# Optimization experiments

Measured on AMD Instinct MI355X. Metric: run time of the kernel, lower is better.

Reference implementation:

```python
import jax, jax.numpy as jnp
import numpy as np
import math

N_HEAD = 9
N_KV_HEAD = 3
HEAD_DIM = 64
ROPE_THETA = 100000.0


def _rope_cos_sin(seq_len, dim, theta):
    inv_freq = 1.0 / (theta ** (jnp.arange(0, dim, 2, dtype=jnp.float32) / dim))  # (dim//2,)
    t = jnp.arange(seq_len, dtype=jnp.float32)
    ang = jnp.outer(t, inv_freq)  # (T, dim//2)
    return jnp.cos(ang), jnp.sin(ang)


def _apply_rope(x, cos, sin):
    # x: (B, H, T, D); pairs are interleaved along D (torch view_as_complex on (..., D//2, 2))
    B, H, T, D = x.shape
    xr = x.reshape(B, H, T, D // 2, 2)
    x0, x1 = xr[..., 0], xr[..., 1]
    c = cos[None, None, :, :]
    s = sin[None, None, :, :]
    out0 = x0 * c - x1 * s
    out1 = x0 * s + x1 * c
    return jnp.stack([out0, out1], axis=-1).reshape(B, H, T, D)


def setup_inputs() -> dict:
    key = jax.random.key(0)
    ks = jax.random.split(key, 5)
    B, T, C = 4, 2048, 576
    scale_in = 1.0 / math.sqrt(C)
    return {
        "x": jax.random.normal(ks[0], (B, T, C), dtype=jnp.float32),
        "wq": jax.random.normal(ks[1], (N_HEAD * HEAD_DIM, C), dtype=jnp.float32) * scale_in,
        "wk": jax.random.normal(ks[2], (N_KV_HEAD * HEAD_DIM, C), dtype=jnp.float32) * scale_in,
        "wv": jax.random.normal(ks[3], (N_KV_HEAD * HEAD_DIM, C), dtype=jnp.float32) * scale_in,
        "wo": jax.random.normal(ks[4], (C, N_HEAD * HEAD_DIM), dtype=jnp.float32) * scale_in,
    }


def reference(x, wq, wk, wv, wo):
    B, T, C = x.shape
    n_rep = N_HEAD // N_KV_HEAD

    q = (x @ wq.T).reshape(B, T, N_HEAD, HEAD_DIM).transpose(0, 2, 1, 3)      # (B,Hq,T,D)
    k = (x @ wk.T).reshape(B, T, N_KV_HEAD, HEAD_DIM).transpose(0, 2, 1, 3)   # (B,Hkv,T,D)
    v = (x @ wv.T).reshape(B, T, N_KV_HEAD, HEAD_DIM).transpose(0, 2, 1, 3)

    cos, sin = _rope_cos_sin(T, HEAD_DIM, ROPE_THETA)
    q = _apply_rope(q, cos, sin)
    k = _apply_rope(k, cos, sin)

    # GQA: broadcast each KV head across n_rep query heads without materializing copies
    qg = q.reshape(B, N_KV_HEAD, n_rep, T, HEAD_DIM)
    att = jnp.einsum("bgrtd,bgsd->bgrts", qg, k) * (1.0 / math.sqrt(HEAD_DIM))  # (B,Hkv,rep,T,T)
    causal = jnp.tril(jnp.ones((T, T), dtype=bool))
    att = jnp.where(causal[None, None, None, :, :], att, -jnp.inf)
    att = jax.nn.softmax(att, axis=-1)
    y = jnp.einsum("bgrts,bgsd->bgrtd", att, v)                                # (B,Hkv,rep,T,D)
    y = y.reshape(B, N_HEAD, T, HEAD_DIM).transpose(0, 2, 1, 3).reshape(B, T, N_HEAD * HEAD_DIM)
    return y @ wo.T
```

## Files before the change

### kernel.cpp

```cpp
#include <hip/hip_runtime.h>
#include <stdint.h>

typedef __attribute__((ext_vector_type(8))) short bf16x8;
typedef __attribute__((ext_vector_type(16))) float f32x16;

#define MFMA32(a, b, c) __builtin_amdgcn_mfma_f32_32x32x16_bf16(a, b, c, 0, 0, 0)

#define BB 4
#define TT 2048
#define CC 576
#define NH 9
#define NKV 3
#define HD 64
#define MM (BB * TT)
#define NQKV 960

#define QSC 0.18033688011112042f

__device__ __forceinline__ unsigned short f2bf(float f) {
  union { float f; uint32_t u; } v; v.f = f;
  uint32_t u = v.u;
  uint32_t r = (u + 0x7fffu + ((u >> 16) & 1u)) >> 16;
  return (unsigned short)r;
}

__device__ __forceinline__ void gl16(const void* g, void* l) {
  __builtin_amdgcn_global_load_lds(
      (const __attribute__((address_space(1))) unsigned int*)g,
      (__attribute__((address_space(3))) unsigned int*)l, 16, 0, 0);
}

__device__ __forceinline__ float fexp2(float x) {
  float r;
  asm("v_exp_f32 %0, %1" : "=v"(r) : "v"(x));
  return r;
}

__global__ __launch_bounds__(256) void prep_kernel(
    const float* __restrict__ x, const float* __restrict__ wq,
    const float* __restrict__ wk, const float* __restrict__ wv,
    const float* __restrict__ wo,
    unsigned short* __restrict__ xh, unsigned short* __restrict__ wqkv,
    unsigned short* __restrict__ woh, float* __restrict__ tc,
    float* __restrict__ ts) {
  const int NX4 = MM * CC / 4;
  const int NW4 = NQKV * CC / 4;
  const int NO4 = CC * CC / 4;
  const int NT = TT * 32;
  const int total = NX4 + NW4 + NO4 + NT;
  for (int i = blockIdx.x * blockDim.x + threadIdx.x; i < total;
       i += gridDim.x * blockDim.x) {
    if (i < NX4) {
      float4 v = ((const float4*)x)[i];
      ushort4 o;
      o.x = f2bf(v.x); o.y = f2bf(v.y); o.z = f2bf(v.z); o.w = f2bf(v.w);
      ((ushort4*)xh)[i] = o;
    } else if (i < NX4 + NW4) {
      int j = i - NX4;
      int n = (j * 4) / CC;
      const float* src = (n < 576) ? wq + j * 4
                       : (n < 768) ? wk + j * 4 - 576 * CC
                                   : wv + j * 4 - 768 * CC;
      float4 v = *(const float4*)src;
      ushort4 o;
      o.x = f2bf(v.x); o.y = f2bf(v.y); o.z = f2bf(v.z); o.w = f2bf(v.w);
      ((ushort4*)wqkv)[j] = o;
    } else if (i < NX4 + NW4 + NO4) {
      int j = i - NX4 - NW4;
      float4 v = ((const float4*)wo)[j];
      ushort4 o;
      o.x = f2bf(v.x); o.y = f2bf(v.y); o.z = f2bf(v.z); o.w = f2bf(v.w);
      ((ushort4*)woh)[j] = o;
    } else {
      int j = i - NX4 - NW4 - NO4;
      int t = j >> 5, pi = j & 31;
      double invf = pow(100000.0, -(double)(2 * pi) / 64.0);
      double ang = (double)t * invf;
      tc[j] = (float)cos(ang);
      ts[j] = (float)sin(ang);
    }
  }
}

__global__ __launch_bounds__(512, 4) void gemm_qkv(
    const unsigned short* __restrict__ xh, const unsigned short* __restrict__ wqkv,
    const float* __restrict__ tc, const float* __restrict__ ts,
    unsigned short* __restrict__ qb, unsigned short* __restrict__ kst,
    unsigned short* __restrict__ vst) {
  const int l = threadIdx.x & 63, w = threadIdx.x >> 6;
  const int ln = l & 31, hi = l >> 5;
  const int bm = blockIdx.y * 256, bn = blockIdx.x * 64;

  __shared__ unsigned short als[2][16384];
  __shared__ unsigned short bls[2][4096];

  int asrc[4];
#pragma unroll
  for (int i = 0; i < 4; ++i)
    asrc[i] = (bm + w * 32 + i * 8 + (l >> 3)) * CC + ((l & 7) ^ ((l >> 3) & 7)) * 8;
  const int bsrc = (bn + w * 8 + (l >> 3)) * CC + ((l & 7) ^ ((l >> 3) & 7)) * 8;

  f32x16 acc0, acc1;
#pragma unroll
  for (int r = 0; r < 16; ++r) { acc0[r] = 0.f; acc1[r] = 0.f; }

#pragma unroll
  for (int i = 0; i < 4; ++i) gl16(xh + asrc[i], (char*)&als[0][0] + w * 4096 + i * 1024);
  gl16(wqkv + bsrc, (char*)&bls[0][0] + w * 1024);

  int cur = 0;
  for (int t = 0; t < 9; ++t) {
    if (t + 1 < 9) {
      const int k0 = (t + 1) * 64;
#pragma unroll
      for (int i = 0; i < 4; ++i)
        gl16(xh + asrc[i] + k0, (char*)&als[cur ^ 1][0] + w * 4096 + i * 1024);
      gl16(wqkv + bsrc + k0, (char*)&bls[cur ^ 1][0] + w * 1024);
      asm volatile("s_waitcnt vmcnt(5)" ::: "memory");
    } else {
      asm volatile("s_waitcnt vmcnt(0)" ::: "memory");
    }
    __builtin_amdgcn_s_barrier();
    __builtin_amdgcn_sched_barrier(0);

    const char* ab = (const char*)&als[cur][0];
    const char* bb = (const char*)&bls[cur][0];
    __builtin_amdgcn_s_setprio(1);
#pragma unroll
    for (int ks = 0; ks < 4; ++ks) {
      const int ch = (((ks * 2 + hi) ^ (ln & 7)) << 4);
      bf16x8 af = *(const bf16x8*)(ab + (w * 32 + ln) * 128 + ch);
      bf16x8 b0 = *(const bf16x8*)(bb + ln * 128 + ch);
      bf16x8 b1 = *(const bf16x8*)(bb + (32 + ln) * 128 + ch);
      acc0 = MFMA32(af, b0, acc0);
      acc1 = MFMA32(af, b1, acc1);
    }
    __builtin_amdgcn_s_setprio(0);

    __builtin_amdgcn_sched_barrier(0);
    __builtin_amdgcn_s_barrier();
    cur ^= 1;
  }

#pragma unroll
  for (int n32 = 0; n32 < 2; ++n32) {
    const int col = bn + n32 * 32 + ln;
    const int d = col & 63;
#pragma unroll
    for (int r = 0; r < 16; ++r) {
      const int m = bm + w * 32 + (r & 3) + 8 * (r >> 2) + 4 * hi;
      float v = n32 ? acc1[r] : acc0[r];
      float partner = __shfl_xor(v, 1);
      const int bi = m >> 11, t = m & 2047;
      if (col < 768) {
        const int pi = d >> 1;
        const float c = tc[t * 32 + pi], s = ts[t * 32 + pi];
        v = (d & 1) ? (partner * s + v * c) : (v * c - partner * s);
      }
      if (col < 576) {
        const int h = col >> 6;
        qb[(((size_t)bi * NH + h) * TT + t) * HD + d] = f2bf(v * QSC);
      } else if (col < 768) {
        const int h = (col - 576) >> 6;
        const size_t head = (size_t)bi * NKV + h;
        const int tt = t & 63;
        kst[(head * 32 + (t >> 6)) * 4096 + ((d >> 4) * 2 + (tt >> 5)) * 512
            + ((((d >> 3) & 1) << 5) + (tt & 31)) * 8 + (d & 7)] = f2bf(v);
      } else {
        const int h = (col - 768) >> 6;
        const size_t head = (size_t)bi * NKV + h;
        const int tt = t & 63;
        vst[(head * 32 + (t >> 6)) * 4096 + ((tt >> 4) * 2 + (d >> 5)) * 512
            + ((((tt >> 3) & 1) << 5) + (d & 31)) * 8 + (tt & 7)] = f2bf(v);
      }
    }
  }
}

__global__ __launch_bounds__(512, 4) void attn_kernel(
    const unsigned short* __restrict__ qbuf, const unsigned short* __restrict__ kst,
    const unsigned short* __restrict__ vst, unsigned short* __restrict__ yb) {
  const int jx = blockIdx.x, kvh = blockIdx.y, b = blockIdx.z;
  const int j = jx % 13, hr = jx / 13;
  const int h = kvh * 3 + hr;
  const int l = threadIdx.x & 63;
  const int w8 = threadIdx.x >> 6;
  const int g = w8 >> 2;
  const int wq = w8 & 3;
  const int ln = l & 31, hi = l >> 5;
  const size_t head = (size_t)b * NKV + kvh;

  const int qt0 = 15 - j;
  const int qt1 = (j >= 9 && j <= 11) ? (j - 9) : -1;
  const int m0 = qt0 + 1;
  const int m1 = (qt1 >= 0) ? qt1 + 1 : 0;
  const int tot = m0 + m1;

  __shared__ unsigned short kls[2][2][4096];
  __shared__ unsigned short vls[2][2][4096];
  __shared__ float licomb[256];

  const unsigned short* qptr = qbuf + ((size_t)b * NH + h) * TT * HD;
  const int row0 = qt0 * 128 + wq * 32 + ln;
  const int row1 = ((qt1 >= 0) ? qt1 : 0) * 128 + wq * 32 + ln;

  bf16x8 qf0[4], qf1[4], qc[4];
#pragma unroll
  for (int ds = 0; ds < 4; ++ds) {
    qf0[ds] = *(const bf16x8*)(qptr + (size_t)row0 * HD + ds * 16 + hi * 8);
    qf1[ds] = *(const bf16x8*)(qptr + (size_t)row1 * HD + ds * 16 + hi * 8);
  }
  qc[0] = qf0[0]; qc[1] = qf0[1]; qc[2] = qf0[2]; qc[3] = qf0[3];
  int qt_c = qt0, qrow_c = row0, nt_c = m0;

  const char* kgb = (const char*)(kst + head * 32 * 4096);
  const char* vgb = (const char*)(vst + head * 32 * 4096);

  f32x16 o0, o1, fzero;
  float ls[16];
#pragma unroll
  for (int r = 0; r < 16; ++r) { o0[r] = 0.f; o1[r] = 0.f; ls[r] = 0.f; fzero[r] = 0.f; }

  {
    const size_t tb = (size_t)g * 8192;
#pragma unroll
    for (int i2 = 0; i2 < 2; ++i2) {
      const int off = wq * 2048 + i2 * 1024;
      gl16(kgb + tb + off + l * 16, (char*)&kls[g][0][0] + off);
      gl16(vgb + tb + off + l * 16, (char*)&vls[g][0][0] + off);
    }
  }

  int jt = 0;

  for (int it = 0; it < tot; ++it) {
    if (it + 1 < tot) {
      const int f = it + 1;
      const int u = (f < m0) ? f : f - m0;
      const size_t tb = (size_t)(2 * u + g) * 8192;
      char* kl = (char*)&kls[g][(it + 1) & 1][0];
      char* vl = (char*)&vls[g][(it + 1) & 1][0];
#pragma unroll
      for (int i2 = 0; i2 < 2; ++i2) {
        const int off = wq * 2048 + i2 * 1024;
        gl16(kgb + tb + off + l * 16, kl + off);
        gl16(vgb + tb + off + l * 16, vl + off);
      }
      asm volatile("s_waitcnt vmcnt(4)" ::: "memory");
    } else {
      asm volatile("s_waitcnt vmcnt(0)" ::: "memory");
    }
    __builtin_amdgcn_s_barrier();
    __builtin_amdgcn_sched_barrier(0);

    const char* kb = (const char*)&kls[g][it & 1][0];
    const char* vb = (const char*)&vls[g][it & 1][0];

    f32x16 s0, s1;
    __builtin_amdgcn_s_setprio(1);
    {
      bf16x8 k0 = *(const bf16x8*)(kb + 0 * 1024 + l * 16);
      bf16x8 k1 = *(const bf16x8*)(kb + 1 * 1024 + l * 16);
      s0 = MFMA32(k0, qc[0], fzero);
      s1 = MFMA32(k1, qc[0], fzero);
    }
#pragma unroll
    for (int ds = 1; ds < 4; ++ds) {
      bf16x8 k0 = *(const bf16x8*)(kb + (ds * 2 + 0) * 1024 + l * 16);
      bf16x8 k1 = *(const bf16x8*)(kb + (ds * 2 + 1) * 1024 + l * 16);
      s0 = MFMA32(k0, qc[ds], s0);
      s1 = MFMA32(k1, qc[ds], s1);
    }
    __builtin_amdgcn_s_setprio(0);

    const bool segEnd = (jt == qt_c);
    if (segEnd) {
      const int kvt = 2 * qt_c + g;
#pragma unroll
      for (int r = 0; r < 16; ++r) {
        const int kg = kvt * 64 + (r & 3) + 8 * (r >> 2) + 4 * hi;
        if (kg > qrow_c) s0[r] = -1e30f;
        if (kg + 32 > qrow_c) s1[r] = -1e30f;
      }
    }

#pragma unroll
    for (int r = 0; r < 16; ++r) {
      s0[r] = fexp2(s0[r]);
      s1[r] = fexp2(s1[r]);
    }
#pragma unroll
    for (int r = 0; r < 16; ++r) ls[r] += s0[r] + s1[r];

    unsigned int pa[4][4];
#pragma unroll
    for (int t = 0; t < 2; ++t) {
#pragma unroll
      for (int m = 0; m < 2; ++m) {
        float p0 = t ? s1[8 * m + 0] : s0[8 * m + 0];
        float p1 = t ? s1[8 * m + 1] : s0[8 * m + 1];
        float p2 = t ? s1[8 * m + 2] : s0[8 * m + 2];
        float p3 = t ? s1[8 * m + 3] : s0[8 * m + 3];
        float p4 = t ? s1[8 * m + 4] : s0[8 * m + 4];
        float p5 = t ? s1[8 * m + 5] : s0[8 * m + 5];
        float p6 = t ? s1[8 * m + 6] : s0[8 * m + 6];
        float p7 = t ? s1[8 * m + 7] : s0[8 * m + 7];
        unsigned int w0, w1, w2, w3;
        asm("v_cvt_pk_bf16_f32 %0, %1, %2" : "=v"(w0) : "v"(p0), "v"(p1));
        asm("v_cvt_pk_bf16_f32 %0, %1, %2" : "=v"(w1) : "v"(p2), "v"(p3));
        asm("v_cvt_pk_bf16_f32 %0, %1, %2" : "=v"(w2) : "v"(p4), "v"(p5));
        asm("v_cvt_pk_bf16_f32 %0, %1, %2" : "=v"(w3) : "v"(p6), "v"(p7));
        asm("v_permlane32_swap_b32 %0, %1" : "+v"(w0), "+v"(w2));
        asm("v_permlane32_swap_b32 %0, %1" : "+v"(w1), "+v"(w3));
        pa[2 * t + m][0] = w0; pa[2 * t + m][1] = w1;
        pa[2 * t + m][2] = w2; pa[2 * t + m][3] = w3;
      }
    }

    __builtin_amdgcn_s_setprio(1);
#pragma unroll
    for (int ks = 0; ks < 4; ++ks) {
      union { unsigned int u[4]; bf16x8 v; } cvt;
      cvt.u[0] = pa[ks][0]; cvt.u[1] = pa[ks][1];
      cvt.u[2] = pa[ks][2]; cvt.u[3] = pa[ks][3];
      bf16x8 v0 = *(const bf16x8*)(vb + (ks * 2 + 0) * 1024 + l * 16);
      bf16x8 v1 = *(const bf16x8*)(vb + (ks * 2 + 1) * 1024 + l * 16);
      o0 = MFMA32(cvt.v, v0, o0);
      o1 = MFMA32(cvt.v, v1, o1);
    }
    __builtin_amdgcn_s_setprio(0);

    if (segEnd) {
#pragma unroll
      for (int st = 8; st >= 1; st >>= 1)
#pragma unroll
        for (int r = 0; r < 8; ++r)
          if (r < st) ls[r] += ls[r + st];
      const float tm0 = ls[0] + __shfl_xor(ls[0], 32);
      char* chunk;
      {
        const int buf = it & 1;
        chunk = (char*)((wq == 0) ? &kls[0][buf][0]
               : (wq == 1) ? &vls[0][buf][0]
               : (wq == 2) ? &kls[1][buf][0]
                           : &vls[1][buf][0]);
      }
      __syncthreads();
      if (g == 1) {
#pragma unroll
        for (int r = 0; r < 16; ++r) {
          *(float*)(chunk + r * 256 + l * 4) = o0[r];
          *(float*)(chunk + (16 + r) * 256 + l * 4) = o1[r];
        }
        licomb[wq * 64 + l] = tm0;
      }
      __syncthreads();
      if (g == 0) {
#pragma unroll
        for (int r = 0; r < 16; ++r) {
          o0[r] += *(const float*)(chunk + r * 256 + l * 4);
          o1[r] += *(const float*)(chunk + (16 + r) * 256 + l * 4);
        }
        const float li = tm0 + licomb[wq * 64 + l];
        const float inv = 1.0f / li;
#pragma unroll
        for (int r = 0; r < 16; ++r) {
          const int cr = (r & 3) + 8 * (r >> 2) + 4 * hi;
          const float ir = __shfl(inv, cr);
          const int t = qt_c * 128 + wq * 32 + cr;
          unsigned short* yp = yb + ((size_t)b * TT + t) * CC + h * HD;
          yp[ln] = f2bf(o0[r] * ir);
          yp[32 + ln] = f2bf(o1[r] * ir);
        }
      }
#pragma unroll
      for (int r = 0; r < 16; ++r) { o0[r] = 0.f; o1[r] = 0.f; ls[r] = 0.f; }
    }

    __builtin_amdgcn_sched_barrier(0);
    __builtin_amdgcn_s_barrier();
    __builtin_amdgcn_sched_barrier(0);

    ++jt;
    if (jt == nt_c && it + 1 < tot) {
      jt = 0;
      qt_c = qt1; qrow_c = row1; nt_c = m1;
      qc[0] = qf1[0]; qc[1] = qf1[1]; qc[2] = qf1[2]; qc[3] = qf1[3];
    }
  }
}

__global__ __launch_bounds__(512, 4) void gemm_out(
    const unsigned short* __restrict__ yb, const unsigned short* __restrict__ woh,
    float* __restrict__ out) {
  const int l = threadIdx.x & 63, w = threadIdx.x >> 6;
  const int ln = l & 31, hi = l >> 5;
  const int bm = blockIdx.y * 256, bn = blockIdx.x * 64;

  __shared__ unsigned short als[2][16384];
  __shared__ unsigned short bls[2][4096];

  int asrc[4];
#pragma unroll
  for (int i = 0; i < 4; ++i)
    asrc[i] = (bm + w * 32 + i * 8 + (l >> 3)) * CC + ((l & 7) ^ ((l >> 3) & 7)) * 8;
  const int bsrc = (bn + w * 8 + (l >> 3)) * CC + ((l & 7) ^ ((l >> 3) & 7)) * 8;

  f32x16 acc0, acc1;
#pragma unroll
  for (int r = 0; r < 16; ++r) { acc0[r] = 0.f; acc1[r] = 0.f; }

#pragma unroll
  for (int i = 0; i < 4; ++i) gl16(yb + asrc[i], (char*)&als[0][0] + w * 4096 + i * 1024);
  gl16(woh + bsrc, (char*)&bls[0][0] + w * 1024);

  int cur = 0;
  for (int t = 0; t < 9; ++t) {
    if (t + 1 < 9) {
      const int k0 = (t + 1) * 64;
#pragma unroll
      for (int i = 0; i < 4; ++i)
        gl16(yb + asrc[i] + k0, (char*)&als[cur ^ 1][0] + w * 4096 + i * 1024);
      gl16(woh + bsrc + k0, (char*)&bls[cur ^ 1][0] + w * 1024);
      asm volatile("s_waitcnt vmcnt(5)" ::: "memory");
    } else {
      asm volatile("s_waitcnt vmcnt(0)" ::: "memory");
    }
    __builtin_amdgcn_s_barrier();
    __builtin_amdgcn_sched_barrier(0);

    const char* ab = (const char*)&als[cur][0];
    const char* bb = (const char*)&bls[cur][0];
    __builtin_amdgcn_s_setprio(1);
#pragma unroll
    for (int ks = 0; ks < 4; ++ks) {
      const int ch = (((ks * 2 + hi) ^ (ln & 7)) << 4);
      bf16x8 af = *(const bf16x8*)(ab + (w * 32 + ln) * 128 + ch);
      bf16x8 b0 = *(const bf16x8*)(bb + ln * 128 + ch);
      bf16x8 b1 = *(const bf16x8*)(bb + (32 + ln) * 128 + ch);
      acc0 = MFMA32(af, b0, acc0);
      acc1 = MFMA32(af, b1, acc1);
    }
    __builtin_amdgcn_s_setprio(0);

    __builtin_amdgcn_sched_barrier(0);
    __builtin_amdgcn_s_barrier();
    cur ^= 1;
  }

#pragma unroll
  for (int n32 = 0; n32 < 2; ++n32) {
    const int col = bn + n32 * 32 + ln;
#pragma unroll
    for (int r = 0; r < 16; ++r) {
      const int m = bm + w * 32 + (r & 3) + 8 * (r >> 2) + 4 * hi;
      out[(size_t)m * CC + col] = n32 ? acc1[r] : acc0[r];
    }
  }
}

extern "C" void kernel_launch(void* const* d_in, const int* in_sizes, int n_in,
                              void* d_out, int out_size, void* d_ws, size_t ws_size,
                              hipStream_t stream) {
  const float* x = (const float*)d_in[0];
  const float* wq = (const float*)d_in[1];
  const float* wk = (const float*)d_in[2];
  const float* wv = (const float*)d_in[3];
  const float* wo = (const float*)d_in[4];
  float* out = (float*)d_out;

  char* ws = (char*)d_ws;
  unsigned short* xh = (unsigned short*)ws;    ws += (size_t)MM * CC * 2;
  unsigned short* wqkv = (unsigned short*)ws;  ws += (size_t)NQKV * CC * 2;
  unsigned short* woh = (unsigned short*)ws;   ws += (size_t)CC * CC * 2;
  float* tc = (float*)ws;                      ws += (size_t)TT * 32 * 4;
  float* tsn = (float*)ws;                     ws += (size_t)TT * 32 * 4;
  unsigned short* qbuf = (unsigned short*)ws;  ws += (size_t)BB * NH * TT * HD * 2;
  unsigned short* kst = (unsigned short*)ws;   ws += (size_t)BB * NKV * TT * HD * 2;
  unsigned short* vst = (unsigned short*)ws;   ws += (size_t)BB * NKV * HD * TT * 2;
  unsigned short* yb = (unsigned short*)ws;    ws += (size_t)MM * CC * 2;

  prep_kernel<<<dim3(2048), dim3(256), 0, stream>>>(x, wq, wk, wv, wo, xh, wqkv, woh, tc, tsn);
  gemm_qkv<<<dim3(NQKV / 64, MM / 256), dim3(512), 0, stream>>>(xh, wqkv, tc, tsn, qbuf, kst, vst);
  attn_kernel<<<dim3(39, NKV, BB), dim3(512), 0, stream>>>(qbuf, kst, vst, yb);
  gemm_out<<<dim3(CC / 64, MM / 256), dim3(512), 0, stream>>>(yb, woh, out);
}
```

Baseline: 98.93 us.

## Split long causal attention rows across blocks with partial-sum epilogue kernel

Replaces the paired query-tile scheduling (one long plus one short tile per block) with a table of 20 bins, where the four longest query tiles (12-15) are split into two KV ranges handled by separate blocks. Split blocks write unnormalized partial outputs and row sums to a scratch buffer aliased over the now-dead xh workspace, and a new epilogue kernel combines and normalizes them. The goal is better load balance and more blocks (720 vs 468) for the causal workload, at the cost of an extra kernel launch and fp32 scratch traffic. The workspace layout is reordered so woh is not overwritten by the scratch.

```diff
diff --git a/kernel.cpp b/kernel.cpp
--- a/kernel.cpp
+++ b/kernel.cpp
@@ -35,6 +35,10 @@
   asm("v_exp_f32 %0, %1" : "=v"(r) : "v"(x));
   return r;
 }
+
+__device__ const signed char BQT[20] = {11,10,9,8,15,15,14,7,14,13,13,12,6,12,5,4,3,2,1,0};
+__device__ const signed char BLO[20] = {0,0,0,0,0,8,0,0,8,0,7,0,0,7,0,0,0,0,0,0};
+__device__ const signed char BHI[20] = {12,11,10,9,8,16,8,8,15,7,14,7,7,13,6,5,4,3,2,1};
 
 __global__ __launch_bounds__(256) void prep_kernel(
     const float* __restrict__ x, const float* __restrict__ wq,
@@ -179,39 +183,30 @@
 
 __global__ __launch_bounds__(512, 4) void attn_kernel(
     const unsigned short* __restrict__ qbuf, const unsigned short* __restrict__ kst,
-    const unsigned short* __restrict__ vst, unsigned short* __restrict__ yb) {
-  const int jx = blockIdx.x, kvh = blockIdx.y, b = blockIdx.z;
-  const int j = jx % 13, hr = jx / 13;
+    const unsigned short* __restrict__ vst, unsigned short* __restrict__ yb,
+    float* __restrict__ pscr) {
+  const int x = blockIdx.x, kvh = blockIdx.y, b = blockIdx.z;
+  const int bin = x / 3, hr = x % 3;
   const int h = kvh * 3 + hr;
+  const int qt = BQT[bin], klo = BLO[bin], khi = BHI[bin];
   const int l = threadIdx.x & 63;
   const int w8 = threadIdx.x >> 6;
   const int g = w8 >> 2;
   const int wq = w8 & 3;
-  const int ln = l & 31, hi = l >> 5;
+  const int ln = l & 31, hb = l >> 5;
   const size_t head = (size_t)b * NKV + kvh;
-
-  const int qt0 = 15 - j;
-  const int qt1 = (j >= 9 && j <= 11) ? (j - 9) : -1;
-  const int m0 = qt0 + 1;
-  const int m1 = (qt1 >= 0) ? qt1 + 1 : 0;
-  const int tot = m0 + m1;
 
   __shared__ unsigned short kls[2][2][4096];
   __shared__ unsigned short vls[2][2][4096];
   __shared__ float licomb[256];
 
   const unsigned short* qptr = qbuf + ((size_t)b * NH + h) * TT * HD;
-  const int row0 = qt0 * 128 + wq * 32 + ln;
-  const int row1 = ((qt1 >= 0) ? qt1 : 0) * 128 + wq * 32 + ln;
-
-  bf16x8 qf0[4], qf1[4], qc[4];
-#pragma unroll
-  for (int ds = 0; ds < 4; ++ds) {
-    qf0[ds] = *(const bf16x8*)(qptr + (size_t)row0 * HD + ds * 16 + hi * 8);
-    qf1[ds] = *(const bf16x8*)(qptr + (size_t)row1 * HD + ds * 16 + hi * 8);
-  }
-  qc[0] = qf0[0]; qc[1] = qf0[1]; qc[2] = qf0[2]; qc[3] = qf0[3];
-  int qt_c = qt0, qrow_c = row0, nt_c = m0;
+  const int qrow = qt * 128 + wq * 32 + ln;
+
+  bf16x8 qc[4];
+#pragma unroll
+  for (int ds = 0; ds < 4; ++ds)
+    qc[ds] = *(const bf16x8*)(qptr + (size_t)qrow * HD + ds * 16 + hb * 8);
 
   const char* kgb = (const char*)(kst + head * 32 * 4096);
   const char* vgb = (const char*)(vst + head * 32 * 4096);
@@ -222,7 +217,7 @@
   for (int r = 0; r < 16; ++r) { o0[r] = 0.f; o1[r] = 0.f; ls[r] = 0.f; fzero[r] = 0.f; }
 
   {
-    const size_t tb = (size_t)g * 8192;
+    const size_t tb = (size_t)(2 * klo + g) * 8192;
 #pragma unroll
     for (int i2 = 0; i2 < 2; ++i2) {
       const int off = wq * 2048 + i2 * 1024;
@@ -231,15 +226,12 @@
     }
   }
 
-  int jt = 0;
-
-  for (int it = 0; it < tot; ++it) {
-    if (it + 1 < tot) {
-      const int f = it + 1;
-      const int u = (f < m0) ? f : f - m0;
-      const size_t tb = (size_t)(2 * u + g) * 8192;
-      char* kl = (char*)&kls[g][(it + 1) & 1][0];
-      char* vl = (char*)&vls[g][(it + 1) & 1][0];
+  for (int u = klo; u < khi; ++u) {
+    const int it2 = u - klo;
+    if (u + 1 < khi) {
+      const size_t tb = (size_t)(2 * (u + 1) + g) * 8192;
+      char* kl = (char*)&kls[g][(it2 + 1) & 1][0];
+      char* vl = (char*)&vls[g][(it2 + 1) & 1][0];
 #pragma unroll
       for (int i2 = 0; i2 < 2; ++i2) {
         const int off = wq * 2048 + i2 * 1024;
@@ -253,8 +245,8 @@
     __builtin_amdgcn_s_barrier();
     __builtin_amdgcn_sched_barrier(0);
 
-    const char* kb = (const char*)&kls[g][it & 1][0];
-    const char* vb = (const char*)&vls[g][it & 1][0];
+    const char* kb = (const char*)&kls[g][it2 & 1][0];
+    const char* vb = (const char*)&vls[g][it2 & 1][0];
 
     f32x16 s0, s1;
     __builtin_amdgcn_s_setprio(1);
@@ -273,14 +265,13 @@
     }
     __builtin_amdgcn_s_setprio(0);
 
-    const bool segEnd = (jt == qt_c);
-    if (segEnd) {
-      const int kvt = 2 * qt_c + g;
+    if (u == qt) {
+      const int kvt = 2 * qt + g;
 #pragma unroll
       for (int r = 0; r < 16; ++r) {
-        const int kg = kvt * 64 + (r & 3) + 8 * (r >> 2) + 4 * hi;
-        if (kg > qrow_c) s0[r] = -1e30f;
-        if (kg + 32 > qrow_c) s1[r] = -1e30f;
+        const int kg = kvt * 64 + (r & 3) + 8 * (r >> 2) + 4 * hb;
+        if (kg > qrow) s0[r] = -1e30f;
+        if (kg + 32 > qrow) s1[r] = -1e30f;
       }
     }
 
@@ -330,63 +321,87 @@
     }
     __builtin_amdgcn_s_setprio(0);
 
-    if (segEnd) {
-#pragma unroll
-      for (int st = 8; st >= 1; st >>= 1)
-#pragma unroll
-        for (int r = 0; r < 8; ++r)
-          if (r < st) ls[r] += ls[r + st];
-      const float tm0 = ls[0] + __shfl_xor(ls[0], 32);
-      char* chunk;
-      {
-        const int buf = it & 1;
-        chunk = (char*)((wq == 0) ? &kls[0][buf][0]
-               : (wq == 1) ? &vls[0][buf][0]
-               : (wq == 2) ? &kls[1][buf][0]
-                           : &vls[1][buf][0]);
-      }
-      __syncthreads();
-      if (g == 1) {
-#pragma unroll
-        for (int r = 0; r < 16; ++r) {
-          *(float*)(chunk + r * 256 + l * 4) = o0[r];
-          *(float*)(chunk + (16 + r) * 256 + l * 4) = o1[r];
-        }
-        licomb[wq * 64 + l] = tm0;
-      }
-      __syncthreads();
-      if (g == 0) {
-#pragma unroll
-        for (int r = 0; r < 16; ++r) {
-          o0[r] += *(const float*)(chunk + r * 256 + l * 4);
-          o1[r] += *(const float*)(chunk + (16 + r) * 256 + l * 4);
-        }
-        const float li = tm0 + licomb[wq * 64 + l];
-        const float inv = 1.0f / li;
-#pragma unroll
-        for (int r = 0; r < 16; ++r) {
-          const int cr = (r & 3) + 8 * (r >> 2) + 4 * hi;
-          const float ir = __shfl(inv, cr);
-          const int t = qt_c * 128 + wq * 32 + cr;
-          unsigned short* yp = yb + ((size_t)b * TT + t) * CC + h * HD;
-          yp[ln] = f2bf(o0[r] * ir);
-          yp[32 + ln] = f2bf(o1[r] * ir);
-        }
-      }
-#pragma unroll
-      for (int r = 0; r < 16; ++r) { o0[r] = 0.f; o1[r] = 0.f; ls[r] = 0.f; }
-    }
-
     __builtin_amdgcn_sched_barrier(0);
     __builtin_amdgcn_s_barrier();
     __builtin_amdgcn_sched_barrier(0);
-
-    ++jt;
-    if (jt == nt_c && it + 1 < tot) {
-      jt = 0;
-      qt_c = qt1; qrow_c = row1; nt_c = m1;
-      qc[0] = qf1[0]; qc[1] = qf1[1]; qc[2] = qf1[2]; qc[3] = qf1[3];
-    }
+  }
+
+#pragma unroll
+  for (int st = 8; st >= 1; st >>= 1)
+#pragma unroll
+    for (int r = 0; r < 8; ++r)
+      if (r < st) ls[r] += ls[r + st];
+  const float tm0 = ls[0] + __shfl_xor(ls[0], 32);
+  char* chunk;
+  {
+    const int buf = (khi - 1 - klo) & 1;
+    chunk = (char*)((wq == 0) ? &kls[0][buf][0]
+           : (wq == 1) ? &vls[0][buf][0]
+           : (wq == 2) ? &kls[1][buf][0]
+                       : &vls[1][buf][0]);
+  }
+  __syncthreads();
+  if (g == 1) {
+#pragma unroll
+    for (int r = 0; r < 16; ++r) {
+      *(float*)(chunk + r * 256 + l * 4) = o0[r];
+      *(float*)(chunk + (16 + r) * 256 + l * 4) = o1[r];
+    }
+    licomb[wq * 64 + l] = tm0;
+  }
+  __syncthreads();
+  if (g == 0) {
+#pragma unroll
+    for (int r = 0; r < 16; ++r) {
+      o0[r] += *(const float*)(chunk + r * 256 + l * 4);
+      o1[r] += *(const float*)(chunk + (16 + r) * 256 + l * 4);
+    }
+    const float li = tm0 + licomb[wq * 64 + l];
+    if (qt >= 12) {
+      const int half = (klo == 0) ? 0 : 1;
+      float* po = pscr + ((((size_t)(b * NH + h) * 4 + (qt - 12)) * 2 + half)) * 8320;
+#pragma unroll
+      for (int r = 0; r < 16; ++r) {
+        const int cr = (r & 3) + 8 * (r >> 2) + 4 * hb;
+        po[(wq * 32 + cr) * 64 + ln] = o0[r];
+        po[(wq * 32 + cr) * 64 + 32 + ln] = o1[r];
+      }
+      if (hb == 0) po[8192 + wq * 32 + ln] = li;
+    } else {
+      const float inv = 1.0f / li;
+#pragma unroll
+      for (int r = 0; r < 16; ++r) {
+        const int cr = (r & 3) + 8 * (r >> 2) + 4 * hb;
+        const float ir = __shfl(inv, cr);
+        const int t = qt * 128 + wq * 32 + cr;
+        unsigned short* yp = yb + ((size_t)b * TT + t) * CC + h * HD;
+        yp[ln] = f2bf(o0[r] * ir);
+        yp[32 + ln] = f2bf(o1[r] * ir);
+      }
+    }
+  }
+}
+
+__global__ __launch_bounds__(256) void attn_epilogue(
+    const float* __restrict__ pscr, unsigned short* __restrict__ yb) {
+  const int q4 = blockIdx.x, h = blockIdx.y, b = blockIdx.z;
+  const int qt = q4 + 12;
+  const float* p0 = pscr + (((size_t)(b * NH + h) * 4 + q4) * 2 + 0) * 8320;
+  const float* p1 = p0 + 8320;
+#pragma unroll
+  for (int e = 0; e < 8; ++e) {
+    const int i4 = e * 256 + threadIdx.x;
+    const int row = i4 >> 4;
+    const float inv = 1.0f / (p0[8192 + row] + p1[8192 + row]);
+    float4 a = ((const float4*)p0)[i4];
+    float4 c = ((const float4*)p1)[i4];
+    ushort4 o;
+    o.x = f2bf((a.x + c.x) * inv);
+    o.y = f2bf((a.y + c.y) * inv);
+    o.z = f2bf((a.z + c.z) * inv);
+    o.w = f2bf((a.w + c.w) * inv);
+    const int col = (i4 & 15) * 4;
+    *(ushort4*)(yb + ((size_t)b * TT + qt * 128 + row) * CC + h * HD + col) = o;
   }
 }
 
@@ -470,11 +485,12 @@
   float* out = (float*)d_out;
 
   char* ws = (char*)d_ws;
+  float* pscr = (float*)d_ws;
   unsigned short* xh = (unsigned short*)ws;    ws += (size_t)MM * CC * 2;
   unsigned short* wqkv = (unsigned short*)ws;  ws += (size_t)NQKV * CC * 2;
-  unsigned short* woh = (unsigned short*)ws;   ws += (size_t)CC * CC * 2;
   float* tc = (float*)ws;                      ws += (size_t)TT * 32 * 4;
   float* tsn = (float*)ws;                     ws += (size_t)TT * 32 * 4;
+  unsigned short* woh = (unsigned short*)ws;   ws += (size_t)CC * CC * 2;
   unsigned short* qbuf = (unsigned short*)ws;  ws += (size_t)BB * NH * TT * HD * 2;
   unsigned short* kst = (unsigned short*)ws;   ws += (size_t)BB * NKV * TT * HD * 2;
   unsigned short* vst = (unsigned short*)ws;   ws += (size_t)BB * NKV * HD * TT * 2;
@@ -482,6 +498,7 @@
 
   prep_kernel<<<dim3(2048), dim3(256), 0, stream>>>(x, wq, wk, wv, wo, xh, wqkv, woh, tc, tsn);
   gemm_qkv<<<dim3(NQKV / 64, MM / 256), dim3(512), 0, stream>>>(xh, wqkv, tc, tsn, qbuf, kst, vst);
-  attn_kernel<<<dim3(39, NKV, BB), dim3(512), 0, stream>>>(qbuf, kst, vst, yb);
+  attn_kernel<<<dim3(60, NKV, BB), dim3(512), 0, stream>>>(qbuf, kst, vst, yb, pscr);
+  attn_epilogue<<<dim3(4, NH, BB), dim3(256), 0, stream>>>(pscr, yb);
   gemm_out<<<dim3(CC / 64, MM / 256), dim3(512), 0, stream>>>(yb, woh, out);
 }
```

Result: slower. 102.6 us (+3.8%).

## Simplify attention to one query tile per block with single KV stream

Applied to the files above, without the earlier changes.

Replaces the two-group split-KV attention blocks, which paired query tiles for load balancing and merged partial outputs through shared memory, with 256-thread blocks that each own one 128-row query tile and walk all KV tiles serially. Per-wave causal skipping avoids computing tiles fully above the diagonal, and the cross-group LDS reduction and extra syncs are removed. The cost is less intra-block KV parallelism and causal load imbalance across blocks, now left to the hardware scheduler with a larger grid of 576 blocks. Workspace buffer order is also shuffled.

```diff
diff --git a/kernel.cpp b/kernel.cpp
--- a/kernel.cpp
+++ b/kernel.cpp
@@ -177,41 +177,27 @@
   }
 }
 
-__global__ __launch_bounds__(512, 4) void attn_kernel(
+__global__ __launch_bounds__(256, 5) void attn_kernel(
     const unsigned short* __restrict__ qbuf, const unsigned short* __restrict__ kst,
     const unsigned short* __restrict__ vst, unsigned short* __restrict__ yb) {
-  const int jx = blockIdx.x, kvh = blockIdx.y, b = blockIdx.z;
-  const int j = jx % 13, hr = jx / 13;
-  const int h = kvh * 3 + hr;
-  const int l = threadIdx.x & 63;
-  const int w8 = threadIdx.x >> 6;
-  const int g = w8 >> 2;
-  const int wq = w8 & 3;
-  const int ln = l & 31, hi = l >> 5;
+  const int qt = 15 - blockIdx.x, h = blockIdx.y, b = blockIdx.z;
+  const int l = threadIdx.x & 63, wq = threadIdx.x >> 6;
+  const int ln = l & 31, hb = l >> 5;
+  const int kvh = h / 3;
   const size_t head = (size_t)b * NKV + kvh;
-
-  const int qt0 = 15 - j;
-  const int qt1 = (j >= 9 && j <= 11) ? (j - 9) : -1;
-  const int m0 = qt0 + 1;
-  const int m1 = (qt1 >= 0) ? qt1 + 1 : 0;
-  const int tot = m0 + m1;
-
-  __shared__ unsigned short kls[2][2][4096];
-  __shared__ unsigned short vls[2][2][4096];
-  __shared__ float licomb[256];
+  const int nt = 2 * qt + 2;
+
+  __shared__ unsigned short kls[2][4096];
+  __shared__ unsigned short vls[2][4096];
 
   const unsigned short* qptr = qbuf + ((size_t)b * NH + h) * TT * HD;
-  const int row0 = qt0 * 128 + wq * 32 + ln;
-  const int row1 = ((qt1 >= 0) ? qt1 : 0) * 128 + wq * 32 + ln;
-
-  bf16x8 qf0[4], qf1[4], qc[4];
-#pragma unroll
-  for (int ds = 0; ds < 4; ++ds) {
-    qf0[ds] = *(const bf16x8*)(qptr + (size_t)row0 * HD + ds * 16 + hi * 8);
-    qf1[ds] = *(const bf16x8*)(qptr + (size_t)row1 * HD + ds * 16 + hi * 8);
-  }
-  qc[0] = qf0[0]; qc[1] = qf0[1]; qc[2] = qf0[2]; qc[3] = qf0[3];
-  int qt_c = qt0, qrow_c = row0, nt_c = m0;
+  const int qrow = qt * 128 + wq * 32 + ln;
+  const int wmax = qt * 128 + wq * 32 + 31;
+
+  bf16x8 qc[4];
+#pragma unroll
+  for (int ds = 0; ds < 4; ++ds)
+    qc[ds] = *(const bf16x8*)(qptr + (size_t)qrow * HD + ds * 16 + hb * 8);
 
   const char* kgb = (const char*)(kst + head * 32 * 4096);
   const char* vgb = (const char*)(vst + head * 32 * 4096);
@@ -221,25 +207,18 @@
 #pragma unroll
   for (int r = 0; r < 16; ++r) { o0[r] = 0.f; o1[r] = 0.f; ls[r] = 0.f; fzero[r] = 0.f; }
 
-  {
-    const size_t tb = (size_t)g * 8192;
-#pragma unroll
-    for (int i2 = 0; i2 < 2; ++i2) {
-      const int off = wq * 2048 + i2 * 1024;
-      gl16(kgb + tb + off + l * 16, (char*)&kls[g][0][0] + off);
-      gl16(vgb + tb + off + l * 16, (char*)&vls[g][0][0] + off);
-    }
-  }
-
-  int jt = 0;
-
-  for (int it = 0; it < tot; ++it) {
-    if (it + 1 < tot) {
-      const int f = it + 1;
-      const int u = (f < m0) ? f : f - m0;
-      const size_t tb = (size_t)(2 * u + g) * 8192;
-      char* kl = (char*)&kls[g][(it + 1) & 1][0];
-      char* vl = (char*)&vls[g][(it + 1) & 1][0];
+#pragma unroll
+  for (int i2 = 0; i2 < 2; ++i2) {
+    const int off = wq * 2048 + i2 * 1024;
+    gl16(kgb + off + l * 16, (char*)&kls[0][0] + off);
+    gl16(vgb + off + l * 16, (char*)&vls[0][0] + off);
+  }
+
+  for (int u = 0; u < nt; ++u) {
+    if (u + 1 < nt) {
+      const size_t tb = (size_t)(u + 1) * 8192;
+      char* kl = (char*)&kls[(u + 1) & 1][0];
+      char* vl = (char*)&vls[(u + 1) & 1][0];
 #pragma unroll
       for (int i2 = 0; i2 < 2; ++i2) {
         const int off = wq * 2048 + i2 * 1024;
@@ -253,140 +232,103 @@
     __builtin_amdgcn_s_barrier();
     __builtin_amdgcn_sched_barrier(0);
 
-    const char* kb = (const char*)&kls[g][it & 1][0];
-    const char* vb = (const char*)&vls[g][it & 1][0];
-
-    f32x16 s0, s1;
-    __builtin_amdgcn_s_setprio(1);
-    {
-      bf16x8 k0 = *(const bf16x8*)(kb + 0 * 1024 + l * 16);
-      bf16x8 k1 = *(const bf16x8*)(kb + 1 * 1024 + l * 16);
-      s0 = MFMA32(k0, qc[0], fzero);
-      s1 = MFMA32(k1, qc[0], fzero);
-    }
-#pragma unroll
-    for (int ds = 1; ds < 4; ++ds) {
-      bf16x8 k0 = *(const bf16x8*)(kb + (ds * 2 + 0) * 1024 + l * 16);
-      bf16x8 k1 = *(const bf16x8*)(kb + (ds * 2 + 1) * 1024 + l * 16);
-      s0 = MFMA32(k0, qc[ds], s0);
-      s1 = MFMA32(k1, qc[ds], s1);
-    }
-    __builtin_amdgcn_s_setprio(0);
-
-    const bool segEnd = (jt == qt_c);
-    if (segEnd) {
-      const int kvt = 2 * qt_c + g;
+    if (64 * u <= wmax) {
+      const char* kb = (const char*)&kls[u & 1][0];
+      const char* vb = (const char*)&vls[u & 1][0];
+
+      f32x16 s0, s1;
+      __builtin_amdgcn_s_setprio(1);
+      {
+        bf16x8 k0 = *(const bf16x8*)(kb + 0 * 1024 + l * 16);
+        bf16x8 k1 = *(const bf16x8*)(kb + 1 * 1024 + l * 16);
+        s0 = MFMA32(k0, qc[0], fzero);
+        s1 = MFMA32(k1, qc[0], fzero);
+      }
+#pragma unroll
+      for (int ds = 1; ds < 4; ++ds) {
+        bf16x8 k0 = *(const bf16x8*)(kb + (ds * 2 + 0) * 1024 + l * 16);
+        bf16x8 k1 = *(const bf16x8*)(kb + (ds * 2 + 1) * 1024 + l * 16);
+        s0 = MFMA32(k0, qc[ds], s0);
+        s1 = MFMA32(k1, qc[ds], s1);
+      }
+      __builtin_amdgcn_s_setprio(0);
+
+      if (u >= 2 * qt) {
+#pragma unroll
+        for (int r = 0; r < 16; ++r) {
+          const int kg = u * 64 + (r & 3) + 8 * (r >> 2) + 4 * hb;
+          if (kg > qrow) s0[r] = -1e30f;
+          if (kg + 32 > qrow) s1[r] = -1e30f;
+        }
+      }
+
 #pragma unroll
       for (int r = 0; r < 16; ++r) {
-        const int kg = kvt * 64 + (r & 3) + 8 * (r >> 2) + 4 * hi;
-        if (kg > qrow_c) s0[r] = -1e30f;
-        if (kg + 32 > qrow_c) s1[r] = -1e30f;
-      }
-    }
-
-#pragma unroll
-    for (int r = 0; r < 16; ++r) {
-      s0[r] = fexp2(s0[r]);
-      s1[r] = fexp2(s1[r]);
-    }
-#pragma unroll
-    for (int r = 0; r < 16; ++r) ls[r] += s0[r] + s1[r];
-
-    unsigned int pa[4][4];
-#pragma unroll
-    for (int t = 0; t < 2; ++t) {
-#pragma unroll
-      for (int m = 0; m < 2; ++m) {
-        float p0 = t ? s1[8 * m + 0] : s0[8 * m + 0];
-        float p1 = t ? s1[8 * m + 1] : s0[8 * m + 1];
-        float p2 = t ? s1[8 * m + 2] : s0[8 * m + 2];
-        float p3 = t ? s1[8 * m + 3] : s0[8 * m + 3];
-        float p4 = t ? s1[8 * m + 4] : s0[8 * m + 4];
-        float p5 = t ? s1[8 * m + 5] : s0[8 * m + 5];
-        float p6 = t ? s1[8 * m + 6] : s0[8 * m + 6];
-        float p7 = t ? s1[8 * m + 7] : s0[8 * m + 7];
-        unsigned int w0, w1, w2, w3;
-        asm("v_cvt_pk_bf16_f32 %0, %1, %2" : "=v"(w0) : "v"(p0), "v"(p1));
-        asm("v_cvt_pk_bf16_f32 %0, %1, %2" : "=v"(w1) : "v"(p2), "v"(p3));
-        asm("v_cvt_pk_bf16_f32 %0, %1, %2" : "=v"(w2) : "v"(p4), "v"(p5));
-        asm("v_cvt_pk_bf16_f32 %0, %1, %2" : "=v"(w3) : "v"(p6), "v"(p7));
-        asm("v_permlane32_swap_b32 %0, %1" : "+v"(w0), "+v"(w2));
-        asm("v_permlane32_swap_b32 %0, %1" : "+v"(w1), "+v"(w3));
-        pa[2 * t + m][0] = w0; pa[2 * t + m][1] = w1;
-        pa[2 * t + m][2] = w2; pa[2 * t + m][3] = w3;
-      }
-    }
-
-    __builtin_amdgcn_s_setprio(1);
-#pragma unroll
-    for (int ks = 0; ks < 4; ++ks) {
-      union { unsigned int u[4]; bf16x8 v; } cvt;
-      cvt.u[0] = pa[ks][0]; cvt.u[1] = pa[ks][1];
-      cvt.u[2] = pa[ks][2]; cvt.u[3] = pa[ks][3];
-      bf16x8 v0 = *(const bf16x8*)(vb + (ks * 2 + 0) * 1024 + l * 16);
-      bf16x8 v1 = *(const bf16x8*)(vb + (ks * 2 + 1) * 1024 + l * 16);
-      o0 = MFMA32(cvt.v, v0, o0);
-      o1 = MFMA32(cvt.v, v1, o1);
-    }
-    __builtin_amdgcn_s_setprio(0);
-
-    if (segEnd) {
-#pragma unroll
-      for (int st = 8; st >= 1; st >>= 1)
-#pragma unroll
-        for (int r = 0; r < 8; ++r)
-          if (r < st) ls[r] += ls[r + st];
-      const float tm0 = ls[0] + __shfl_xor(ls[0], 32);
-      char* chunk;
-      {
-        const int buf = it & 1;
-        chunk = (char*)((wq == 0) ? &kls[0][buf][0]
-               : (wq == 1) ? &vls[0][buf][0]
-               : (wq == 2) ? &kls[1][buf][0]
-                           : &vls[1][buf][0]);
-      }
-      __syncthreads();
-      if (g == 1) {
-#pragma unroll
-        for (int r = 0; r < 16; ++r) {
-          *(float*)(chunk + r * 256 + l * 4) = o0[r];
-          *(float*)(chunk + (16 + r) * 256 + l * 4) = o1[r];
+        s0[r] = fexp2(s0[r]);
+        s1[r] = fexp2(s1[r]);
+      }
+#pragma unroll
+      for (int r = 0; r < 16; ++r) ls[r] += s0[r] + s1[r];
+
+      unsigned int pa[4][4];
+#pragma unroll
+      for (int t = 0; t < 2; ++t) {
+#pragma unroll
+        for (int m = 0; m < 2; ++m) {
+          float p0 = t ? s1[8 * m + 0] : s0[8 * m + 0];
+          float p1 = t ? s1[8 * m + 1] : s0[8 * m + 1];
+          float p2 = t ? s1[8 * m + 2] : s0[8 * m + 2];
+          float p3 = t ? s1[8 * m + 3] : s0[8 * m + 3];
+          float p4 = t ? s1[8 * m + 4] : s0[8 * m + 4];
+          float p5 = t ? s1[8 * m + 5] : s0[8 * m + 5];
+          float p6 = t ? s1[8 * m + 6] : s0[8 * m + 6];
+          float p7 = t ? s1[8 * m + 7] : s0[8 * m + 7];
+          unsigned int w0, w1, w2, w3;
+          asm("v_cvt_pk_bf16_f32 %0, %1, %2" : "=v"(w0) : "v"(p0), "v"(p1));
+          asm("v_cvt_pk_bf16_f32 %0, %1, %2" : "=v"(w1) : "v"(p2), "v"(p3));
+          asm("v_cvt_pk_bf16_f32 %0, %1, %2" : "=v"(w2) : "v"(p4), "v"(p5));
+          asm("v_cvt_pk_bf16_f32 %0, %1, %2" : "=v"(w3) : "v"(p6), "v"(p7));
+          asm("v_permlane32_swap_b32 %0, %1" : "+v"(w0), "+v"(w2));
+          asm("v_permlane32_swap_b32 %0, %1" : "+v"(w1), "+v"(w3));
+          pa[2 * t + m][0] = w0; pa[2 * t + m][1] = w1;
+          pa[2 * t + m][2] = w2; pa[2 * t + m][3] = w3;
         }
-        licomb[wq * 64 + l] = tm0;
-      }
-      __syncthreads();
-      if (g == 0) {
-#pragma unroll
-        for (int r = 0; r < 16; ++r) {
-          o0[r] += *(const float*)(chunk + r * 256 + l * 4);
-          o1[r] += *(const float*)(chunk + (16 + r) * 256 + l * 4);
-        }
-        const float li = tm0 + licomb[wq * 64 + l];
-        const float inv = 1.0f / li;
-#pragma unroll
-        for (int r = 0; r < 16; ++r) {
-          const int cr = (r & 3) + 8 * (r >> 2) + 4 * hi;
-          const float ir = __shfl(inv, cr);
-          const int t = qt_c * 128 + wq * 32 + cr;
-          unsigned short* yp = yb + ((size_t)b * TT + t) * CC + h * HD;
-          yp[ln] = f2bf(o0[r] * ir);
-          yp[32 + ln] = f2bf(o1[r] * ir);
-        }
-      }
-#pragma unroll
-      for (int r = 0; r < 16; ++r) { o0[r] = 0.f; o1[r] = 0.f; ls[r] = 0.f; }
-    }
-
-    __builtin_amdgcn_sched_barrier(0);
-    __builtin_amdgcn_s_barrier();
-    __builtin_amdgcn_sched_barrier(0);
-
-    ++jt;
-    if (jt == nt_c && it + 1 < tot) {
-      jt = 0;
-      qt_c = qt1; qrow_c = row1; nt_c = m1;
-      qc[0] = qf1[0]; qc[1] = qf1[1]; qc[2] = qf1[2]; qc[3] = qf1[3];
-    }
+      }
+
+      __builtin_amdgcn_s_setprio(1);
+#pragma unroll
+      for (int ks = 0; ks < 4; ++ks) {
+        union { unsigned int u[4]; bf16x8 v; } cvt;
+        cvt.u[0] = pa[ks][0]; cvt.u[1] = pa[ks][1];
+        cvt.u[2] = pa[ks][2]; cvt.u[3] = pa[ks][3];
+        bf16x8 v0 = *(const bf16x8*)(vb + (ks * 2 + 0) * 1024 + l * 16);
+        bf16x8 v1 = *(const bf16x8*)(vb + (ks * 2 + 1) * 1024 + l * 16);
+        o0 = MFMA32(cvt.v, v0, o0);
+        o1 = MFMA32(cvt.v, v1, o1);
+      }
+      __builtin_amdgcn_s_setprio(0);
+    }
+
+    __builtin_amdgcn_sched_barrier(0);
+    __builtin_amdgcn_s_barrier();
+    __builtin_amdgcn_sched_barrier(0);
+  }
+
+#pragma unroll
+  for (int st = 8; st >= 1; st >>= 1)
+#pragma unroll
+    for (int r = 0; r < 8; ++r)
+      if (r < st) ls[r] += ls[r + st];
+  const float li = ls[0] + __shfl_xor(ls[0], 32);
+  const float inv = 1.0f / li;
+#pragma unroll
+  for (int r = 0; r < 16; ++r) {
+    const int cr = (r & 3) + 8 * (r >> 2) + 4 * hb;
+    const float ir = __shfl(inv, cr);
+    const int t = qt * 128 + wq * 32 + cr;
+    unsigned short* yp = yb + ((size_t)b * TT + t) * CC + h * HD;
+    yp[ln] = f2bf(o0[r] * ir);
+    yp[32 + ln] = f2bf(o1[r] * ir);
   }
 }
 
@@ -472,9 +414,9 @@
   char* ws = (char*)d_ws;
   unsigned short* xh = (unsigned short*)ws;    ws += (size_t)MM * CC * 2;
   unsigned short* wqkv = (unsigned short*)ws;  ws += (size_t)NQKV * CC * 2;
-  unsigned short* woh = (unsigned short*)ws;   ws += (size_t)CC * CC * 2;
   float* tc = (float*)ws;                      ws += (size_t)TT * 32 * 4;
   float* tsn = (float*)ws;                     ws += (size_t)TT * 32 * 4;
+  unsigned short* woh = (unsigned short*)ws;   ws += (size_t)CC * CC * 2;
   unsigned short* qbuf = (unsigned short*)ws;  ws += (size_t)BB * NH * TT * HD * 2;
   unsigned short* kst = (unsigned short*)ws;   ws += (size_t)BB * NKV * TT * HD * 2;
   unsigned short* vst = (unsigned short*)ws;   ws += (size_t)BB * NKV * HD * TT * 2;
@@ -482,6 +424,6 @@
 
   prep_kernel<<<dim3(2048), dim3(256), 0, stream>>>(x, wq, wk, wv, wo, xh, wqkv, woh, tc, tsn);
   gemm_qkv<<<dim3(NQKV / 64, MM / 256), dim3(512), 0, stream>>>(xh, wqkv, tc, tsn, qbuf, kst, vst);
-  attn_kernel<<<dim3(39, NKV, BB), dim3(512), 0, stream>>>(qbuf, kst, vst, yb);
+  attn_kernel<<<dim3(16, NH, BB), dim3(256), 0, stream>>>(qbuf, kst, vst, yb);
   gemm_out<<<dim3(CC / 64, MM / 256), dim3(512), 0, stream>>>(yb, woh, out);
 }
```

Measured after the change: 145.7 us. 47.3% more time.
